# Performance work log

Measured on AMD Instinct MI355X. Metric: run time of the kernel, lower is better.

## Reference

```python
import jax, jax.numpy as jnp
import numpy as np

N_NODES = 100000
N_EDGES = 800000
IN_DIM, HID_DIM, OUT_DIM = 128, 64, 7


def setup_inputs() -> dict:
    key = jax.random.key(0)
    ks = jax.random.split(key, 8)
    x = jax.random.normal(ks[0], (N_NODES, IN_DIM), dtype=jnp.float32)
    edge_index = jax.random.randint(ks[1], (2, N_EDGES), 0, N_NODES, dtype=jnp.int64)
    # Glorot-ish init for weights, zeros for bias (PyG GCNConv default)
    def glorot(k, shape):
        lim = float(np.sqrt(6.0 / (shape[0] + shape[1])))
        return jax.random.uniform(k, shape, dtype=jnp.float32, minval=-lim, maxval=lim)
    return {
        "x": x,
        "edge_index": edge_index,
        "W1": glorot(ks[2], (IN_DIM, HID_DIM)),
        "b1": jnp.zeros((HID_DIM,), jnp.float32),
        "W2": glorot(ks[3], (HID_DIM, HID_DIM)),
        "b2": jnp.zeros((HID_DIM,), jnp.float32),
        "W3": glorot(ks[4], (HID_DIM, OUT_DIM)),
        "b3": jnp.zeros((OUT_DIM,), jnp.float32),
    }


def _gcn_conv(h_in, src, dst, W, b, n_nodes):
    # PyG GCNConv: h = x @ W; add self-loops; D^-1/2 A_hat D^-1/2 aggregation; + b
    h = h_in @ W  # [N, F_out]
    # degree over destination nodes, +1 for self-loop
    deg = jax.ops.segment_sum(jnp.ones_like(dst, dtype=h.dtype), dst,
                              num_segments=n_nodes) + 1.0
    dinv = jax.lax.rsqrt(deg)  # [N]
    coef = dinv[src] * dinv[dst]  # [E]
    msg = h[src] * coef[:, None]  # gather + scale  [E, F_out]
    out = jax.ops.segment_sum(msg, dst, num_segments=n_nodes)  # scatter-add
    out = out + h * (dinv * dinv)[:, None]  # self-loop contribution
    return out + b


def reference(x, edge_index, W1, b1, W2, b2, W3, b3):
    src, dst = edge_index[0], edge_index[1]
    n = x.shape[0]
    h = jax.nn.relu(_gcn_conv(x, src, dst, W1, b1, n))
    # dropout(p=0.5) is identity in eval mode
    h = jax.nn.relu(_gcn_conv(h, src, dst, W2, b2, n))
    return _gcn_conv(h, src, dst, W3, b3, n)
```

## Files before the change

kernel.cpp:

```cpp
#include <hip/hip_runtime.h>

#define N_NODES 100000
#define N_EDGES 800000
#define IN_DIM 128
#define HID 64
#define OUT_DIM 7
#define CAP 32
#define NGROUP 8
#define DSLICE (N_NODES / NGROUP)
#define SUBBLK 390

typedef __bf16 vbf8 __attribute__((ext_vector_type(8)));
typedef float  vf4  __attribute__((ext_vector_type(4)));

#define GEMM_BLKS ((N_NODES / 16 + 3) / 4)
#define FILL_BLKS (NGROUP * SUBBLK)
#define PH1_BLKS (GEMM_BLKS + FILL_BLKS)

__device__ __forceinline__ void wswz_body(int idx, const float* __restrict__ W,
                                          __bf16* __restrict__ out) {
    int j  = idx & 7;
    int l  = (idx >> 3) & 63;
    int nt = (idx >> 9) & 3;
    int ks = idx >> 11;
    int k  = ks * 32 + ((l >> 4) << 3) + j;
    int n  = nt * 16 + (l & 15);
    out[idx] = (__bf16)W[k * 64 + n];
}

__global__ __launch_bounds__(256)
void k_init(const float* __restrict__ W1, __bf16* __restrict__ Wz1,
            const float* __restrict__ W2, __bf16* __restrict__ Wz2,
            int* __restrict__ cnt,
            __bf16* __restrict__ HbA, __bf16* __restrict__ HbB,
            float* __restrict__ S) {
    int b = blockIdx.x;
    int t = threadIdx.x;
    if (b < 32) { wswz_body(b * 256 + t, W1, Wz1); return; }
    if (b < 48) { wswz_body((b - 32) * 256 + t, W2, Wz2); return; }
    if (b < 147) {
        int idx = (b - 48) * 256 + t;
        if (idx < 25000)      ((int4*)cnt)[idx] = make_int4(0, 0, 0, 0);
        else if (idx == 25000) cnt[N_NODES] = 0;
        return;
    }
    if (t < 32)       ((unsigned*)(HbA + (size_t)N_NODES * 64))[t] = 0u;
    else if (t < 64)  ((unsigned*)(HbB + (size_t)N_NODES * 64))[t - 32] = 0u;
    else if (t < 71)  S[(size_t)N_NODES * 7 + (t - 64)] = 0.0f;
}

__device__ __forceinline__ void gemm1_body(int g, int tid, const float* __restrict__ X,
                                           const __bf16* __restrict__ Wswz,
                                           __bf16* __restrict__ Hb) {
    constexpr int K = IN_DIM, KS = K / 32;
    const int lane = tid & 63;
    const int w = g * 4 + (tid >> 6);
    if (w >= N_NODES / 16) return;
    const int r0 = w * 16;
    const int m = lane & 15;
    const int quad = lane >> 4;

    vbf8 bfrag[KS][4];
    const vbf8* wp = (const vbf8*)Wswz;
    #pragma unroll
    for (int ks = 0; ks < KS; ++ks)
        #pragma unroll
        for (int nt = 0; nt < 4; ++nt)
            bfrag[ks][nt] = wp[(ks * 4 + nt) * 64 + lane];

    vf4 acc[4] = {};
    #pragma unroll
    for (int ks = 0; ks < KS; ++ks) {
        const float* xp = X + (size_t)(r0 + m) * K + ks * 32 + quad * 8;
        float4 f0 = *(const float4*)xp;
        float4 f1 = *(const float4*)(xp + 4);
        vbf8 a;
        a[0] = (__bf16)f0.x; a[1] = (__bf16)f0.y; a[2] = (__bf16)f0.z; a[3] = (__bf16)f0.w;
        a[4] = (__bf16)f1.x; a[5] = (__bf16)f1.y; a[6] = (__bf16)f1.z; a[7] = (__bf16)f1.w;
        #pragma unroll
        for (int nt = 0; nt < 4; ++nt)
            acc[nt] = __builtin_amdgcn_mfma_f32_16x16x32_bf16(a, bfrag[ks][nt], acc[nt], 0, 0, 0);
    }
    #pragma unroll
    for (int nt = 0; nt < 4; ++nt)
        #pragma unroll
        for (int r = 0; r < 4; ++r)
            Hb[(size_t)(r0 + quad * 4 + r) * 64 + nt * 16 + m] = (__bf16)acc[nt][r];
}

__device__ __forceinline__ void fill_body(int bb, int tid, const int* __restrict__ ei,
                                          int* __restrict__ cnt, int* __restrict__ csr) {
    int group = bb & 7, sub = bb >> 3;
    int lo = group * DSLICE;
    const int4* dst4 = (const int4*)(ei + N_EDGES);
    const int4* src4 = (const int4*)ei;
    for (int e4 = sub * 256 + tid; e4 < N_EDGES / 4; e4 += SUBBLK * 256) {
        int4 d4 = dst4[e4];
        bool m0 = (unsigned)(d4.x - lo) < (unsigned)DSLICE;
        bool m1 = (unsigned)(d4.y - lo) < (unsigned)DSLICE;
        bool m2 = (unsigned)(d4.z - lo) < (unsigned)DSLICE;
        bool m3 = (unsigned)(d4.w - lo) < (unsigned)DSLICE;
        if (!(m0 | m1 | m2 | m3)) continue;
        int4 s4 = src4[e4];
        int p0 = 0, p1 = 0, p2 = 0, p3 = 0;
        if (m0) p0 = atomicAdd(&cnt[d4.x], 1);
        if (m1) p1 = atomicAdd(&cnt[d4.y], 1);
        if (m2) p2 = atomicAdd(&cnt[d4.z], 1);
        if (m3) p3 = atomicAdd(&cnt[d4.w], 1);
        if (m0 && p0 < CAP) csr[(size_t)d4.x * CAP + p0] = s4.x;
        if (m1 && p1 < CAP) csr[(size_t)d4.y * CAP + p1] = s4.y;
        if (m2 && p2 < CAP) csr[(size_t)d4.z * CAP + p2] = s4.z;
        if (m3 && p3 < CAP) csr[(size_t)d4.w * CAP + p3] = s4.w;
    }
}

__global__ __launch_bounds__(256)
void k_phase1(const int* __restrict__ ei, int* __restrict__ cnt, int* __restrict__ csr,
              const float* __restrict__ X, const __bf16* __restrict__ Wz1,
              __bf16* __restrict__ HbA) {
    int b = blockIdx.x;
    if (b < GEMM_BLKS) gemm1_body(b, threadIdx.x, X, Wz1, HbA);
    else               fill_body(b - GEMM_BLKS, threadIdx.x, ei, cnt, csr);
}

__global__ __launch_bounds__(256)
void k_g64gemm2(const int* __restrict__ cnt, const int* __restrict__ csr,
                const float* __restrict__ bias, const __bf16* __restrict__ Hs,
                const __bf16* __restrict__ Wz2, __bf16* __restrict__ HbB) {
    __shared__ __bf16 tl[32][72];
    const int tid = threadIdx.x;
    const int nl = tid >> 3;
    const int q  = tid & 7;
    const int node = blockIdx.x * 32 + nl;

    int deg = cnt[node];
    int end = deg < CAP ? deg : CAP;
    float dd = rsqrtf((float)deg + 1.0f);
    vbf8 h8 = *(const vbf8*)(Hs + (size_t)node * 64 + q * 8);
    float acc[8];
    #pragma unroll
    for (int t = 0; t < 8; ++t) acc[t] = (float)h8[t] * dd;

    const int4* row4 = (const int4*)(csr + (size_t)node * CAP);
    int4 qa = row4[0], qb = row4[1], qc = row4[2], qd = row4[3];
    int srcs[16] = {qa.x, qa.y, qa.z, qa.w, qb.x, qb.y, qb.z, qb.w,
                    qc.x, qc.y, qc.z, qc.w, qd.x, qd.y, qd.z, qd.w};
    #pragma unroll
    for (int t = 0; t < 16; ++t) {
        int s = (t < end) ? srcs[t] : N_NODES;
        float ds = rsqrtf((float)cnt[s] + 1.0f);
        vbf8 v = *(const vbf8*)(Hs + (size_t)s * 64 + q * 8);
        #pragma unroll
        for (int u = 0; u < 8; ++u) acc[u] += (float)v[u] * ds;
    }
    for (int j = 16; j < end; ++j) {
        int s = (csr + (size_t)node * CAP)[j];
        float ds = rsqrtf((float)cnt[s] + 1.0f);
        vbf8 v = *(const vbf8*)(Hs + (size_t)s * 64 + q * 8);
        #pragma unroll
        for (int u = 0; u < 8; ++u) acc[u] += (float)v[u] * ds;
    }
    float4 b0 = *(const float4*)(bias + q * 8);
    float4 b1 = *(const float4*)(bias + q * 8 + 4);
    float bb[8] = {b0.x, b0.y, b0.z, b0.w, b1.x, b1.y, b1.z, b1.w};
    vbf8 o;
    #pragma unroll
    for (int t = 0; t < 8; ++t) o[t] = (__bf16)fmaxf(fmaf(acc[t], dd, bb[t]), 0.f);
    *(vbf8*)&tl[nl][q * 8] = o;
    __syncthreads();

    const int wave = tid >> 6;
    const int lane = tid & 63;
    const int m = lane & 15;
    const int quad = lane >> 4;
    const int tile = wave >> 1;
    const int nt0 = (wave & 1) * 2;

    vbf8 bfrag[2][2];
    const vbf8* wp = (const vbf8*)Wz2;
    #pragma unroll
    for (int ks = 0; ks < 2; ++ks)
        #pragma unroll
        for (int i = 0; i < 2; ++i)
            bfrag[ks][i] = wp[(ks * 4 + nt0 + i) * 64 + lane];

    vf4 acc2[2] = {};
    #pragma unroll
    for (int ks = 0; ks < 2; ++ks) {
        vbf8 a = *(const vbf8*)&tl[tile * 16 + m][ks * 32 + quad * 8];
        #pragma unroll
        for (int i = 0; i < 2; ++i)
            acc2[i] = __builtin_amdgcn_mfma_f32_16x16x32_bf16(a, bfrag[ks][i], acc2[i], 0, 0, 0);
    }
    const int gr0 = blockIdx.x * 32 + tile * 16;
    float dv[4];
    #pragma unroll
    for (int r = 0; r < 4; ++r)
        dv[r] = rsqrtf((float)cnt[gr0 + quad * 4 + r] + 1.0f);
    #pragma unroll
    for (int i = 0; i < 2; ++i)
        #pragma unroll
        for (int r = 0; r < 4; ++r)
            HbB[(size_t)(gr0 + quad * 4 + r) * 64 + (nt0 + i) * 16 + m] =
                (__bf16)(acc2[i][r] * dv[r]);
}

__global__ __launch_bounds__(256)
void k_gather64m(const int* __restrict__ cnt, const int* __restrict__ csr,
                 const float* __restrict__ bias, const __bf16* __restrict__ Hs,
                 const float* __restrict__ W3, float* __restrict__ S) {
    int node = blockIdx.x * 32 + (threadIdx.x >> 3);
    int q = threadIdx.x & 7;
    if (node >= N_NODES) return;
    int deg = cnt[node];
    int end = deg < CAP ? deg : CAP;
    float dd = rsqrtf((float)deg + 1.0f);
    vbf8 h8 = *(const vbf8*)(Hs + (size_t)node * 64 + q * 8);
    float acc[8];
    #pragma unroll
    for (int t = 0; t < 8; ++t) acc[t] = (float)h8[t];

    const int4* row4 = (const int4*)(csr + (size_t)node * CAP);
    int4 qa = row4[0], qb = row4[1], qc = row4[2], qd = row4[3];
    int srcs[16] = {qa.x, qa.y, qa.z, qa.w, qb.x, qb.y, qb.z, qb.w,
                    qc.x, qc.y, qc.z, qc.w, qd.x, qd.y, qd.z, qd.w};
    #pragma unroll
    for (int t = 0; t < 16; ++t) {
        int s = (t < end) ? srcs[t] : N_NODES;
        vbf8 v = *(const vbf8*)(Hs + (size_t)s * 64 + q * 8);
        #pragma unroll
        for (int u = 0; u < 8; ++u) acc[u] += (float)v[u];
    }
    for (int j = 16; j < end; ++j) {
        int s = (csr + (size_t)node * CAP)[j];
        vbf8 v = *(const vbf8*)(Hs + (size_t)s * 64 + q * 8);
        #pragma unroll
        for (int u = 0; u < 8; ++u) acc[u] += (float)v[u];
    }

    float4 b0 = *(const float4*)(bias + q * 8);
    float4 b1 = *(const float4*)(bias + q * 8 + 4);
    float bb[8] = {b0.x, b0.y, b0.z, b0.w, b1.x, b1.y, b1.z, b1.w};
    float p[7] = {};
    #pragma unroll
    for (int t = 0; t < 8; ++t) {
        float r = fmaxf(fmaf(acc[t], dd, bb[t]), 0.f);
        #pragma unroll
        for (int j = 0; j < 7; ++j)
            p[j] = fmaf(r, W3[(q * 8 + t) * 7 + j], p[j]);
    }
    #pragma unroll
    for (int msk = 1; msk < 8; msk <<= 1)
        #pragma unroll
        for (int j = 0; j < 7; ++j)
            p[j] += __shfl_xor(p[j], msk, 8);
    if (q < 7) {
        float v = p[0];
        if (q == 1) v = p[1]; else if (q == 2) v = p[2]; else if (q == 3) v = p[3];
        else if (q == 4) v = p[4]; else if (q == 5) v = p[5]; else if (q == 6) v = p[6];
        S[(size_t)node * 7 + q] = v * dd;
    }
}

__global__ __launch_bounds__(256)
void k_gather7(const int* __restrict__ cnt, const int* __restrict__ csr,
               const float* __restrict__ S, const float* __restrict__ b3,
               float* __restrict__ Out) {
    int node = blockIdx.x * 32 + (threadIdx.x >> 3);
    int j7 = threadIdx.x & 7;
    if (node >= N_NODES || j7 >= 7) return;
    int deg = cnt[node];
    int end = deg < CAP ? deg : CAP;
    float dd = rsqrtf((float)deg + 1.0f);
    const int4* row4 = (const int4*)(csr + (size_t)node * CAP);
    int4 qa = row4[0], qb = row4[1], qc = row4[2], qd = row4[3];
    int srcs[16] = {qa.x, qa.y, qa.z, qa.w, qb.x, qb.y, qb.z, qb.w,
                    qc.x, qc.y, qc.z, qc.w, qd.x, qd.y, qd.z, qd.w};
    float acc = S[(size_t)node * 7 + j7];
    #pragma unroll
    for (int t = 0; t < 16; ++t) {
        int s = (t < end) ? srcs[t] : N_NODES;
        acc += S[(size_t)s * 7 + j7];
    }
    for (int j = 16; j < end; ++j) {
        int s = (csr + (size_t)node * CAP)[j];
        acc += S[(size_t)s * 7 + j7];
    }
    Out[(size_t)node * 7 + j7] = fmaf(acc, dd, b3[j7]);
}

static inline size_t align256(size_t x) { return (x + 255) & ~(size_t)255; }

extern "C" void kernel_launch(void* const* d_in, const int* in_sizes, int n_in,
                              void* d_out, int out_size, void* d_ws, size_t ws_size,
                              hipStream_t stream) {
    const float* x  = (const float*)d_in[0];
    const int*   ei = (const int*)d_in[1];
    const float* W1 = (const float*)d_in[2];
    const float* b1 = (const float*)d_in[3];
    const float* W2 = (const float*)d_in[4];
    const float* b2 = (const float*)d_in[5];
    const float* W3 = (const float*)d_in[6];
    const float* b3 = (const float*)d_in[7];
    float* out = (float*)d_out;

    char* wsp = (char*)d_ws;
    int*    cnt  = (int*)wsp;    wsp += align256(sizeof(int) * (N_NODES + 1));
    int*    csr  = (int*)wsp;    wsp += align256(sizeof(int) * (size_t)N_NODES * CAP);
    __bf16* Wz1  = (__bf16*)wsp; wsp += align256(sizeof(__bf16) * IN_DIM * 64);
    __bf16* Wz2  = (__bf16*)wsp; wsp += align256(sizeof(__bf16) * HID * 64);
    __bf16* HbA  = (__bf16*)wsp; wsp += align256(sizeof(__bf16) * (size_t)(N_NODES + 1) * 64);
    __bf16* HbB  = (__bf16*)wsp; wsp += align256(sizeof(__bf16) * (size_t)(N_NODES + 1) * 64);
    float*  bufS = (float*)wsp;  wsp += align256(sizeof(float) * (size_t)(N_NODES + 1) * 7);

    k_init<<<148, 256, 0, stream>>>(W1, Wz1, W2, Wz2, cnt, HbA, HbB, bufS);
    k_phase1<<<PH1_BLKS, 256, 0, stream>>>(ei, cnt, csr, x, Wz1, HbA);
    k_g64gemm2<<<N_NODES / 32, 256, 0, stream>>>(cnt, csr, b1, HbA, Wz2, HbB);
    k_gather64m<<<N_NODES / 32, 256, 0, stream>>>(cnt, csr, b2, HbB, W3, bufS);
    k_gather7<<<N_NODES / 32, 256, 0, stream>>>(cnt, csr, bufS, b3, out);
}
```

Measured before the change: 199.4 us.

## Prescale layer-1 features by dinv and batch gather loads with tree reductions

Adds a separate k_scale pass that multiplies the layer-1 bf16 features by each node's inverse-sqrt degree. This removes the per-edge cnt lookup and rsqrt from the layer-2 gather. The three gather kernels now issue all 16 neighbor loads up front and sum them with a tree reduction, which raises memory-level parallelism. Launch bounds hint at 2 blocks per SM, and phase1 puts the fill blocks first. The cost is an extra kernel launch, a full read-write pass over HbA, and one more bf16 rounding step.

```diff
diff --git a/kernel.cpp b/kernel.cpp
--- a/kernel.cpp
+++ b/kernel.cpp
@@ -119,11 +119,22 @@
               const float* __restrict__ X, const __bf16* __restrict__ Wz1,
               __bf16* __restrict__ HbA) {
     int b = blockIdx.x;
-    if (b < GEMM_BLKS) gemm1_body(b, threadIdx.x, X, Wz1, HbA);
-    else               fill_body(b - GEMM_BLKS, threadIdx.x, ei, cnt, csr);
+    if (b < FILL_BLKS) fill_body(b, threadIdx.x, ei, cnt, csr);
+    else               gemm1_body(b - FILL_BLKS, threadIdx.x, X, Wz1, HbA);
 }
 
 __global__ __launch_bounds__(256)
+void k_scale(const int* __restrict__ cnt, __bf16* __restrict__ Hb) {
+    int idx = (blockIdx.x * 256 + threadIdx.x) * 8;
+    int row = idx >> 6;
+    float dinv = rsqrtf((float)cnt[row] + 1.0f);
+    vbf8 v = *(const vbf8*)(Hb + idx);
+    #pragma unroll
+    for (int t = 0; t < 8; ++t) v[t] = (__bf16)((float)v[t] * dinv);
+    *(vbf8*)(Hb + idx) = v;
+}
+
+__global__ __launch_bounds__(256, 2)
 void k_g64gemm2(const int* __restrict__ cnt, const int* __restrict__ csr,
                 const float* __restrict__ bias, const __bf16* __restrict__ Hs,
                 const __bf16* __restrict__ Wz2, __bf16* __restrict__ HbB) {
@@ -136,29 +147,34 @@
     int deg = cnt[node];
     int end = deg < CAP ? deg : CAP;
     float dd = rsqrtf((float)deg + 1.0f);
-    vbf8 h8 = *(const vbf8*)(Hs + (size_t)node * 64 + q * 8);
-    float acc[8];
-    #pragma unroll
-    for (int t = 0; t < 8; ++t) acc[t] = (float)h8[t] * dd;
 
     const int4* row4 = (const int4*)(csr + (size_t)node * CAP);
     int4 qa = row4[0], qb = row4[1], qc = row4[2], qd = row4[3];
     int srcs[16] = {qa.x, qa.y, qa.z, qa.w, qb.x, qb.y, qb.z, qb.w,
                     qc.x, qc.y, qc.z, qc.w, qd.x, qd.y, qd.z, qd.w};
+    vbf8 v[16];
     #pragma unroll
     for (int t = 0; t < 16; ++t) {
         int s = (t < end) ? srcs[t] : N_NODES;
-        float ds = rsqrtf((float)cnt[s] + 1.0f);
-        vbf8 v = *(const vbf8*)(Hs + (size_t)s * 64 + q * 8);
-        #pragma unroll
-        for (int u = 0; u < 8; ++u) acc[u] += (float)v[u] * ds;
-    }
+        v[t] = *(const vbf8*)(Hs + (size_t)s * 64 + q * 8);
+    }
+    vbf8 h8 = *(const vbf8*)(Hs + (size_t)node * 64 + q * 8);
+    float a4[4][8];
+    #pragma unroll
+    for (int g = 0; g < 4; ++g)
+        #pragma unroll
+        for (int u = 0; u < 8; ++u)
+            a4[g][u] = ((float)v[g * 4][u] + (float)v[g * 4 + 1][u])
+                     + ((float)v[g * 4 + 2][u] + (float)v[g * 4 + 3][u]);
+    float acc[8];
+    #pragma unroll
+    for (int u = 0; u < 8; ++u)
+        acc[u] = ((a4[0][u] + a4[1][u]) + (a4[2][u] + a4[3][u])) + (float)h8[u];
     for (int j = 16; j < end; ++j) {
         int s = (csr + (size_t)node * CAP)[j];
-        float ds = rsqrtf((float)cnt[s] + 1.0f);
-        vbf8 v = *(const vbf8*)(Hs + (size_t)s * 64 + q * 8);
-        #pragma unroll
-        for (int u = 0; u < 8; ++u) acc[u] += (float)v[u] * ds;
+        vbf8 w = *(const vbf8*)(Hs + (size_t)s * 64 + q * 8);
+        #pragma unroll
+        for (int u = 0; u < 8; ++u) acc[u] += (float)w[u];
     }
     float4 b0 = *(const float4*)(bias + q * 8);
     float4 b1 = *(const float4*)(bias + q * 8 + 4);
@@ -205,7 +221,7 @@
                 (__bf16)(acc2[i][r] * dv[r]);
 }
 
-__global__ __launch_bounds__(256)
+__global__ __launch_bounds__(256, 2)
 void k_gather64m(const int* __restrict__ cnt, const int* __restrict__ csr,
                  const float* __restrict__ bias, const __bf16* __restrict__ Hs,
                  const float* __restrict__ W3, float* __restrict__ S) {
@@ -215,27 +231,34 @@
     int deg = cnt[node];
     int end = deg < CAP ? deg : CAP;
     float dd = rsqrtf((float)deg + 1.0f);
-    vbf8 h8 = *(const vbf8*)(Hs + (size_t)node * 64 + q * 8);
-    float acc[8];
-    #pragma unroll
-    for (int t = 0; t < 8; ++t) acc[t] = (float)h8[t];
 
     const int4* row4 = (const int4*)(csr + (size_t)node * CAP);
     int4 qa = row4[0], qb = row4[1], qc = row4[2], qd = row4[3];
     int srcs[16] = {qa.x, qa.y, qa.z, qa.w, qb.x, qb.y, qb.z, qb.w,
                     qc.x, qc.y, qc.z, qc.w, qd.x, qd.y, qd.z, qd.w};
+    vbf8 v[16];
     #pragma unroll
     for (int t = 0; t < 16; ++t) {
         int s = (t < end) ? srcs[t] : N_NODES;
-        vbf8 v = *(const vbf8*)(Hs + (size_t)s * 64 + q * 8);
-        #pragma unroll
-        for (int u = 0; u < 8; ++u) acc[u] += (float)v[u];
-    }
+        v[t] = *(const vbf8*)(Hs + (size_t)s * 64 + q * 8);
+    }
+    vbf8 h8 = *(const vbf8*)(Hs + (size_t)node * 64 + q * 8);
+    float a4[4][8];
+    #pragma unroll
+    for (int g = 0; g < 4; ++g)
+        #pragma unroll
+        for (int u = 0; u < 8; ++u)
+            a4[g][u] = ((float)v[g * 4][u] + (float)v[g * 4 + 1][u])
+                     + ((float)v[g * 4 + 2][u] + (float)v[g * 4 + 3][u]);
+    float acc[8];
+    #pragma unroll
+    for (int u = 0; u < 8; ++u)
+        acc[u] = ((a4[0][u] + a4[1][u]) + (a4[2][u] + a4[3][u])) + (float)h8[u];
     for (int j = 16; j < end; ++j) {
         int s = (csr + (size_t)node * CAP)[j];
-        vbf8 v = *(const vbf8*)(Hs + (size_t)s * 64 + q * 8);
-        #pragma unroll
-        for (int u = 0; u < 8; ++u) acc[u] += (float)v[u];
+        vbf8 w = *(const vbf8*)(Hs + (size_t)s * 64 + q * 8);
+        #pragma unroll
+        for (int u = 0; u < 8; ++u) acc[u] += (float)w[u];
     }
 
     float4 b0 = *(const float4*)(bias + q * 8);
@@ -255,10 +278,10 @@
         for (int j = 0; j < 7; ++j)
             p[j] += __shfl_xor(p[j], msk, 8);
     if (q < 7) {
-        float v = p[0];
-        if (q == 1) v = p[1]; else if (q == 2) v = p[2]; else if (q == 3) v = p[3];
-        else if (q == 4) v = p[4]; else if (q == 5) v = p[5]; else if (q == 6) v = p[6];
-        S[(size_t)node * 7 + q] = v * dd;
+        float v2 = p[0];
+        if (q == 1) v2 = p[1]; else if (q == 2) v2 = p[2]; else if (q == 3) v2 = p[3];
+        else if (q == 4) v2 = p[4]; else if (q == 5) v2 = p[5]; else if (q == 6) v2 = p[6];
+        S[(size_t)node * 7 + q] = v2 * dd;
     }
 }
 
@@ -276,12 +299,16 @@
     int4 qa = row4[0], qb = row4[1], qc = row4[2], qd = row4[3];
     int srcs[16] = {qa.x, qa.y, qa.z, qa.w, qb.x, qb.y, qb.z, qb.w,
                     qc.x, qc.y, qc.z, qc.w, qd.x, qd.y, qd.z, qd.w};
-    float acc = S[(size_t)node * 7 + j7];
+    float v[16];
     #pragma unroll
     for (int t = 0; t < 16; ++t) {
         int s = (t < end) ? srcs[t] : N_NODES;
-        acc += S[(size_t)s * 7 + j7];
-    }
+        v[t] = S[(size_t)s * 7 + j7];
+    }
+    float self = S[(size_t)node * 7 + j7];
+    float acc = (((v[0] + v[1]) + (v[2] + v[3])) + ((v[4] + v[5]) + (v[6] + v[7])))
+              + (((v[8] + v[9]) + (v[10] + v[11])) + ((v[12] + v[13]) + (v[14] + v[15])))
+              + self;
     for (int j = 16; j < end; ++j) {
         int s = (csr + (size_t)node * CAP)[j];
         acc += S[(size_t)s * 7 + j7];
@@ -315,6 +342,7 @@
 
     k_init<<<148, 256, 0, stream>>>(W1, Wz1, W2, Wz2, cnt, HbA, HbB, bufS);
     k_phase1<<<PH1_BLKS, 256, 0, stream>>>(ei, cnt, csr, x, Wz1, HbA);
+    k_scale<<<(N_NODES * 64) / (8 * 256), 256, 0, stream>>>(cnt, HbA);
     k_g64gemm2<<<N_NODES / 32, 256, 0, stream>>>(cnt, csr, b1, HbA, Wz2, HbB);
     k_gather64m<<<N_NODES / 32, 256, 0, stream>>>(cnt, csr, b2, HbB, W3, bufS);
     k_gather7<<<N_NODES / 32, 256, 0, stream>>>(cnt, csr, bufS, b3, out);
```

Result: no change. 202.3 us (+1.4%).
